# Performance work log

Measured on AMD Instinct MI355X. Metric: run time of the kernel, lower is better.

## Reference

```python
import jax, jax.numpy as jnp
import numpy as np
from jax.scipy.linalg import solve_triangular
from jax.scipy.special import logsumexp

N, K, D = 131072, 32, 32
LOG_2PI = np.float32(np.log(2.0 * np.pi))


def setup_inputs() -> dict:
    key = jax.random.key(0)
    k1, k2, k3, k4 = jax.random.split(key, 4)
    X = jax.random.normal(k1, (N, D), dtype=jnp.float32)
    means = jax.random.normal(k2, (K, D), dtype=jnp.float32)
    chols = jax.random.normal(k3, (K, D, D), dtype=jnp.float32)
    weights = jax.random.normal(k4, (K,), dtype=jnp.float32) - 1.0  # normal_(-1, 1)
    return {"X": X, "means": means, "chols": chols, "weights": weights, "it": 0}


def _neglog_likelihood(X, means, chols, weights):
    d = X.shape[-1]
    n = X.shape[0]
    eye = jnp.eye(d, dtype=X.dtype)
    # sigmas[k] = chols[k] @ chols[k]^T + I  -> (K, D, D)
    sigmas = jnp.einsum('kij,klj->kil', chols, chols) + eye
    L = jnp.linalg.cholesky(sigmas)                      # (K, D, D)
    # per-cluster Gaussian log-densities for all points, batched
    diff = X[None, :, :] - means[:, None, :]             # (K, N, D)
    y = solve_triangular(L, diff.transpose(0, 2, 1), lower=True)  # (K, D, N)
    maha = jnp.sum(y * y, axis=1)                        # (K, N)
    logdet = 2.0 * jnp.sum(jnp.log(jnp.diagonal(L, axis1=-2, axis2=-1)), axis=-1)  # (K,)
    log_dens = -0.5 * (maha + (logdet + d * LOG_2PI)[:, None])    # (K, N)
    dens = jnp.exp(log_dens)                             # (K, N)
    # sum_{i,j} w_i w_j N_i(x) N_j(x) = (sum_k w_k N_k(x))^2
    numer = jnp.square(weights @ dens)                   # (N,)
    # pairwise normaliser Z_ij = N(mu_i; mu_j, S_i + S_j), all pairs batched
    S_ij = sigmas[:, None] + sigmas[None, :]             # (K, K, D, D)
    L_ij = jnp.linalg.cholesky(S_ij)
    dmu = means[:, None, :] - means[None, :, :]          # (K, K, D)
    y_ij = solve_triangular(L_ij, dmu[..., None], lower=True)[..., 0]  # (K, K, D)
    maha_ij = jnp.sum(y_ij * y_ij, axis=-1)              # (K, K)
    logdet_ij = 2.0 * jnp.sum(jnp.log(jnp.diagonal(L_ij, axis1=-2, axis2=-1)), axis=-1)
    Z_ij = jnp.exp(-0.5 * (maha_ij + logdet_ij + d * LOG_2PI))
    z = jnp.sum((weights[:, None] * weights[None, :]) * Z_ij)
    pdf = numer / z                                      # (N,)
    logp = jnp.log(pdf)                                  # (N,)
    return -(logsumexp(logp, axis=0) / n)


def reference(X, means, chols, weights, it):
    return _neglog_likelihood(X, means, chols, weights)
```

## Files before the change

kernel.cpp:

```cpp
#include <hip/hip_runtime.h>
#include <math.h>

#define NPTS  131072
#define NPTB  512
#define NPRB  256
#define GRID  (NPTB + NPRB)
#define DLOG2PIF 58.8120661f
#define DLOG2PI  58.81206612467475
#define SHIFT 92.0f
#define NEGHALF_LOG2E -0.72134752044f
#define LOG2E 1.44269504089f

typedef __attribute__((ext_vector_type(8)))  short short8;
typedef __attribute__((ext_vector_type(16))) float f32x16;

static __device__ __forceinline__ unsigned bfh(float f) {
  unsigned u = __float_as_uint(f);
  return (u + 0x7FFFu + ((u >> 16) & 1u)) >> 16;
}
static __device__ __forceinline__ float bfhf(float f) {
  return __uint_as_float(bfh(f) << 16);
}
static __device__ __forceinline__ short8 mk_a2(unsigned w) {
  int4 t = {(int)w, 0, 0, 0};
  return __builtin_bit_cast(short8, t);
}

__global__ __launch_bounds__(256) void setup_kernel(
    const float* __restrict__ means, const float* __restrict__ chols,
    const float* __restrict__ wts,
    uint4* __restrict__ Afrag, float* __restrict__ Kc, float* __restrict__ Sg,
    unsigned* __restrict__ ticket)
{
  const int tid = threadIdx.x, wv = tid >> 6, lane = tid & 63;
  const int r = lane & 31, h = lane >> 5;
  const int k = blockIdx.x*4 + wv;
  __shared__ float SshA[4][1056];
  __shared__ float blsA[4][1056];
  float* Ssh = SshA[wv];
  float* bls = blsA[wv];
  if (blockIdx.x == 0 && tid == 0) *ticket = 0u;
  const float* cp = chols + (size_t)k*1024 + r*32;
  float4 fa = *(const float4*)(cp + h*8);
  float4 fb = *(const float4*)(cp + h*8 + 4);
  float4 fc = *(const float4*)(cp + 16 + h*8);
  float4 fd = *(const float4*)(cp + 16 + h*8 + 4);
  float v0[8] = {fa.x,fa.y,fa.z,fa.w,fb.x,fb.y,fb.z,fb.w};
  float v1[8] = {fc.x,fc.y,fc.z,fc.w,fd.x,fd.y,fd.z,fd.w};
  short8 hi0, hi1, lo0, lo1;
  #pragma unroll
  for (int j = 0; j < 8; j++) {
    hi0[j] = (short)bfh(v0[j]);  lo0[j] = (short)bfh(v0[j] - bfhf(v0[j]));
    hi1[j] = (short)bfh(v1[j]);  lo1[j] = (short)bfh(v1[j] - bfhf(v1[j]));
  }
  f32x16 acc = {};
  acc = __builtin_amdgcn_mfma_f32_32x32x16_bf16(hi0, hi0, acc, 0,0,0);
  acc = __builtin_amdgcn_mfma_f32_32x32x16_bf16(hi1, hi1, acc, 0,0,0);
  acc = __builtin_amdgcn_mfma_f32_32x32x16_bf16(hi0, lo0, acc, 0,0,0);
  acc = __builtin_amdgcn_mfma_f32_32x32x16_bf16(hi1, lo1, acc, 0,0,0);
  acc = __builtin_amdgcn_mfma_f32_32x32x16_bf16(lo0, hi0, acc, 0,0,0);
  acc = __builtin_amdgcn_mfma_f32_32x32x16_bf16(lo1, hi1, acc, 0,0,0);
  #pragma unroll
  for (int q = 0; q < 16; q++) {
    int row = (q & 3) + 8*(q >> 2) + 4*h;
    Ssh[row*33 + r] = acc[q] + ((row == r) ? 1.0f : 0.0f);
  }
  float a[32];
  #pragma unroll
  for (int j = 0; j < 32; j++) a[j] = Ssh[r*33 + j];
  float ldsum = 0.0f;
  #pragma unroll
  for (int j = 0; j < 32; j++) {
    float dd = __shfl(a[j], j);
    float inv = __frsqrt_rn(dd);
    float sq = dd * inv;
    ldsum += __logf(sq);
    float l = a[j] * inv;
    #pragma unroll
    for (int e = j+1; e < 32; e++) {
      float le = __shfl(l, e);
      a[e] = (r >= e) ? fmaf(-l, le, a[e]) : a[e];
    }
    a[j] = (r == j) ? sq : ((r > j) ? l : a[j]);
  }
  #pragma unroll
  for (int j = 0; j < 32; j++) Ssh[r*33 + j] = a[j];
  #pragma unroll 1
  for (int d = 0; d < 32; d++) {
    float s0 = (d == r) ? 1.0f : 0.0f, s1 = 0.0f;
    int j = 0;
    for (; j + 1 < d; j += 2) {
      s0 = fmaf(-Ssh[d*33 + j],     bls[j*33 + r],     s0);
      s1 = fmaf(-Ssh[d*33 + j + 1], bls[(j+1)*33 + r], s1);
    }
    if (j < d) s0 = fmaf(-Ssh[d*33 + j], bls[j*33 + r], s0);
    bls[d*33 + r] = (s0 + s1) / Ssh[d*33 + d];
  }
  float t0[8], t1[8];
  #pragma unroll
  for (int j = 0; j < 8; j++) {
    t0[j] = bls[r*33 + h*8 + j];
    t1[j] = bls[r*33 + 16 + h*8 + j];
  }
  uint4 s0 = make_uint4(bfh(t0[0])|(bfh(t0[1])<<16), bfh(t0[2])|(bfh(t0[3])<<16),
                        bfh(t0[4])|(bfh(t0[5])<<16), bfh(t0[6])|(bfh(t0[7])<<16));
  uint4 s1 = make_uint4(bfh(t1[0])|(bfh(t1[1])<<16), bfh(t1[2])|(bfh(t1[3])<<16),
                        bfh(t1[4])|(bfh(t1[5])<<16), bfh(t1[6])|(bfh(t1[7])<<16));
  float cvp = 0.0f;
  #pragma unroll
  for (int j = 0; j < 8; j++) {
    cvp = fmaf(t0[j], means[k*32 + h*8 + j], cvp);
    cvp = fmaf(t1[j], means[k*32 + 16 + h*8 + j], cvp);
  }
  float cv = cvp + __shfl_xor(cvp, 32);
  unsigned ch = bfh(cv) ^ 0x8000u;
  unsigned cl = bfh(cv - bfhf(cv)) ^ 0x8000u;
  uint4 s2 = make_uint4((h == 0) ? (ch | (cl<<16)) : 0u, 0u, 0u, 0u);
  Afrag[(k*3 + 0)*64 + lane] = s0;
  Afrag[(k*3 + 1)*64 + lane] = s1;
  Afrag[(k*3 + 2)*64 + lane] = s2;
  if (lane == 0) {
    float wk = wts[k];
    float ld2 = 2.0f*ldsum + DLOG2PIF;
    Kc[k] = LOG2E*(SHIFT - 0.5f*ld2) + log2f(fabsf(wk));
    Sg[k] = (wk < 0.0f) ? -1.0f : 1.0f;
  }
}

__global__ __launch_bounds__(256) void work_kernel(
    const float* __restrict__ X, const float* __restrict__ means,
    const float* __restrict__ chols, const float* __restrict__ wts,
    const uint4* __restrict__ Afrag, const float* __restrict__ Kc,
    const float* __restrict__ Sg,
    double* __restrict__ zterm, double* __restrict__ partials,
    unsigned* __restrict__ ticket, float* __restrict__ out)
{
  __shared__ __align__(16) char smem[24576];
  __shared__ float K2sh[32], sksh[32];
  __shared__ double redd[4], redz[4];
  __shared__ unsigned lastFlag;
  const int tid = threadIdx.x, wv = tid >> 6, lane = tid & 63;
  const int r = lane & 31, h = lane >> 5;
  if (blockIdx.x < NPTB) {
    uint4* fsh = (uint4*)smem;
    const unsigned* fshw = (const unsigned*)smem;
    if (tid < 32) { K2sh[tid] = Kc[tid]; sksh[tid] = Sg[tid]; }
    const int n0 = blockIdx.x*256 + wv*64 + r;
    short8 xh00, xh01, xh10, xh11, x2c;
    {
      const float* xp0 = X + (size_t)n0*32;
      const float* xp1 = X + (size_t)(n0+32)*32;
      float4 fa = *(const float4*)(xp0 + h*8);
      float4 fb = *(const float4*)(xp0 + h*8 + 4);
      float4 fc = *(const float4*)(xp0 + 16 + h*8);
      float4 fd = *(const float4*)(xp0 + 16 + h*8 + 4);
      float4 ga = *(const float4*)(xp1 + h*8);
      float4 gb = *(const float4*)(xp1 + h*8 + 4);
      float4 gc = *(const float4*)(xp1 + 16 + h*8);
      float4 gd = *(const float4*)(xp1 + 16 + h*8 + 4);
      float v00[8] = {fa.x,fa.y,fa.z,fa.w,fb.x,fb.y,fb.z,fb.w};
      float v01[8] = {fc.x,fc.y,fc.z,fc.w,fd.x,fd.y,fd.z,fd.w};
      float v10[8] = {ga.x,ga.y,ga.z,ga.w,gb.x,gb.y,gb.z,gb.w};
      float v11[8] = {gc.x,gc.y,gc.z,gc.w,gd.x,gd.y,gd.z,gd.w};
      #pragma unroll
      for (int j = 0; j < 8; j++) {
        xh00[j] = (short)bfh(v00[j]);  xh01[j] = (short)bfh(v01[j]);
        xh10[j] = (short)bfh(v10[j]);  xh11[j] = (short)bfh(v11[j]);
        x2c[j] = 0;
      }
      if (h == 0) { x2c[0] = (short)0x3F80; x2c[1] = (short)0x3F80; }
    }
    float sF0 = 0.0f, sF1 = 0.0f;
    #pragma unroll 1
    for (int ph = 0; ph < 4; ph++) {
      __syncthreads();
      const uint4* src = Afrag + ph*1536;
      #pragma unroll
      for (int t = tid; t < 1536; t += 256) fsh[t] = src[t];
      __syncthreads();
      #pragma unroll 4
      for (int kk = 0; kk < 8; kk++) {
        const short8* fp = (const short8*)(fsh + kk*192);
        short8 a0 = fp[lane], a1 = fp[64+lane];
        short8 a2 = mk_a2(fshw[(kk*192 + 128 + lane)*4]);
        const int kidx = ph*8 + kk;
        const float Kk = K2sh[kidx], sk = sksh[kidx];
        f32x16 acc0 = {}, acc1 = {};
        acc0 = __builtin_amdgcn_mfma_f32_32x32x16_bf16(a0, xh00, acc0, 0,0,0);
        acc0 = __builtin_amdgcn_mfma_f32_32x32x16_bf16(a1, xh01, acc0, 0,0,0);
        acc0 = __builtin_amdgcn_mfma_f32_32x32x16_bf16(a2, x2c,  acc0, 0,0,0);
        acc1 = __builtin_amdgcn_mfma_f32_32x32x16_bf16(a0, xh10, acc1, 0,0,0);
        acc1 = __builtin_amdgcn_mfma_f32_32x32x16_bf16(a1, xh11, acc1, 0,0,0);
        acc1 = __builtin_amdgcn_mfma_f32_32x32x16_bf16(a2, x2c,  acc1, 0,0,0);
        float m0a=0.f, m0b=0.f, m1a=0.f, m1b=0.f;
        #pragma unroll
        for (int q = 0; q < 8; q++) {
          m0a = fmaf(acc0[q],   acc0[q],   m0a);
          m0b = fmaf(acc0[q+8], acc0[q+8], m0b);
          m1a = fmaf(acc1[q],   acc1[q],   m1a);
          m1b = fmaf(acc1[q+8], acc1[q+8], m1b);
        }
        float m0 = m0a + m0b, m1 = m1a + m1b;
        m0 += __shfl_xor(m0, 32);
        m1 += __shfl_xor(m1, 32);
        sF0 = fmaf(sk, exp2f(fmaf(m0, NEGHALF_LOG2E, Kk)), sF0);
        sF1 = fmaf(sk, exp2f(fmaf(m1, NEGHALF_LOG2E, Kk)), sF1);
      }
    }
    double Tp = (double)sF0*(double)sF0 + (double)sF1*(double)sF1;
    if (lane >= 32) Tp = 0.0;
    #pragma unroll
    for (int off = 32; off > 0; off >>= 1) Tp += __shfl_down(Tp, off);
    if (lane == 0) redd[wv] = Tp;
    __syncthreads();
    if (tid == 0) partials[blockIdx.x] = redd[0] + redd[1] + redd[2] + redd[3];
  } else {
    float* Ssh = (float*)smem + wv*1056;
    const int pid = (blockIdx.x - NPTB)*4 + wv, pi = pid >> 5, pj = pid & 31;
    const float* cpi = chols + (size_t)pi*1024 + r*32;
    const float* cpj = chols + (size_t)pj*1024 + r*32;
    float4 ia = *(const float4*)(cpi + h*8);
    float4 ib = *(const float4*)(cpi + h*8 + 4);
    float4 ic = *(const float4*)(cpi + 16 + h*8);
    float4 id = *(const float4*)(cpi + 16 + h*8 + 4);
    float4 ja = *(const float4*)(cpj + h*8);
    float4 jb = *(const float4*)(cpj + h*8 + 4);
    float4 jc = *(const float4*)(cpj + 16 + h*8);
    float4 jd = *(const float4*)(cpj + 16 + h*8 + 4);
    float vi0[8] = {ia.x,ia.y,ia.z,ia.w,ib.x,ib.y,ib.z,ib.w};
    float vi1[8] = {ic.x,ic.y,ic.z,ic.w,id.x,id.y,id.z,id.w};
    float vj0[8] = {ja.x,ja.y,ja.z,ja.w,jb.x,jb.y,jb.z,jb.w};
    float vj1[8] = {jc.x,jc.y,jc.z,jc.w,jd.x,jd.y,jd.z,jd.w};
    short8 I0h,I0l,I1h,I1l,J0h,J0l,J1h,J1l;
    #pragma unroll
    for (int j = 0; j < 8; j++) {
      I0h[j]=(short)bfh(vi0[j]); I0l[j]=(short)bfh(vi0[j]-bfhf(vi0[j]));
      I1h[j]=(short)bfh(vi1[j]); I1l[j]=(short)bfh(vi1[j]-bfhf(vi1[j]));
      J0h[j]=(short)bfh(vj0[j]); J0l[j]=(short)bfh(vj0[j]-bfhf(vj0[j]));
      J1h[j]=(short)bfh(vj1[j]); J1l[j]=(short)bfh(vj1[j]-bfhf(vj1[j]));
    }
    f32x16 pacc = {};
    pacc = __builtin_amdgcn_mfma_f32_32x32x16_bf16(I0h, I0h, pacc, 0,0,0);
    pacc = __builtin_amdgcn_mfma_f32_32x32x16_bf16(I1h, I1h, pacc, 0,0,0);
    pacc = __builtin_amdgcn_mfma_f32_32x32x16_bf16(I0h, I0l, pacc, 0,0,0);
    pacc = __builtin_amdgcn_mfma_f32_32x32x16_bf16(I1h, I1l, pacc, 0,0,0);
    pacc = __builtin_amdgcn_mfma_f32_32x32x16_bf16(I0l, I0h, pacc, 0,0,0);
    pacc = __builtin_amdgcn_mfma_f32_32x32x16_bf16(I1l, I1h, pacc, 0,0,0);
    pacc = __builtin_amdgcn_mfma_f32_32x32x16_bf16(J0h, J0h, pacc, 0,0,0);
    pacc = __builtin_amdgcn_mfma_f32_32x32x16_bf16(J1h, J1h, pacc, 0,0,0);
    pacc = __builtin_amdgcn_mfma_f32_32x32x16_bf16(J0h, J0l, pacc, 0,0,0);
    pacc = __builtin_amdgcn_mfma_f32_32x32x16_bf16(J1h, J1l, pacc, 0,0,0);
    pacc = __builtin_amdgcn_mfma_f32_32x32x16_bf16(J0l, J0h, pacc, 0,0,0);
    pacc = __builtin_amdgcn_mfma_f32_32x32x16_bf16(J1l, J1h, pacc, 0,0,0);
    #pragma unroll
    for (int q = 0; q < 16; q++) {
      int row = (q & 3) + 8*(q >> 2) + 4*h;
      Ssh[row*33 + r] = pacc[q] + ((row == r) ? 2.0f : 0.0f);
    }
    float a[32];
    #pragma unroll
    for (int j = 0; j < 32; j++) a[j] = Ssh[r*33 + j];
    #pragma unroll
    for (int j = 0; j < 32; j++) {
      float dd = __shfl(a[j], j);
      float inv = __frsqrt_rn(dd);
      float sq = dd * inv;
      float l = a[j] * inv;
      #pragma unroll
      for (int e = j+1; e < 32; e++) {
        float le = __shfl(l, e);
        a[e] = (r >= e) ? fmaf(-l, le, a[e]) : a[e];
      }
      a[j] = (r == j) ? sq : ((r > j) ? l : a[j]);
    }
    float acc2 = means[pi*32 + r] - means[pj*32 + r];
    float maha = 0.0f, ldsum = 0.0f;
    #pragma unroll
    for (int d = 0; d < 32; d++) {
      float dd = __shfl(a[d], d);
      float yd = __shfl(acc2, d) / dd;
      maha = fmaf(yd, yd, maha);
      ldsum += __logf(dd);
      acc2 = (r > d) ? fmaf(-a[d], yd, acc2) : acc2;
    }
    if (lane == 0) {
      double vd = -0.5 * ((double)maha + 2.0*(double)ldsum + DLOG2PI);
      zterm[pid] = (double)wts[pi] * (double)wts[pj] * exp(vd);
    }
  }
  __syncthreads();
  if (tid == 0) {
    __threadfence();
    lastFlag = (atomicAdd(ticket, 1u) == GRID - 1) ? 1u : 0u;
  }
  __syncthreads();
  if (lastFlag) {
    __threadfence();
    double t = 0.0, z = 0.0;
    for (int p = tid; p < NPTB; p += 256) t += partials[p];
    for (int p = tid; p < 1024; p += 256) z += zterm[p];
    #pragma unroll
    for (int off = 32; off > 0; off >>= 1) {
      t += __shfl_down(t, off);
      z += __shfl_down(z, off);
    }
    if (lane == 0) { redd[wv] = t; redz[wv] = z; }
    __syncthreads();
    if (tid == 0) {
      t = redd[0] + redd[1] + redd[2] + redd[3];
      z = redz[0] + redz[1] + redz[2] + redz[3];
      double logT = log(t) - 2.0*(double)SHIFT;
      double logz = log(z);
      out[0] = (float)((logz - logT) / (double)NPTS);
    }
  }
}

extern "C" void kernel_launch(void* const* d_in, const int* in_sizes, int n_in,
                              void* d_out, int out_size, void* d_ws, size_t ws_size,
                              hipStream_t stream) {
  const float* X     = (const float*)d_in[0];
  const float* means = (const float*)d_in[1];
  const float* chols = (const float*)d_in[2];
  const float* wts   = (const float*)d_in[3];
  float* out = (float*)d_out;
  char* ws = (char*)d_ws;
  uint4*    Afrag    = (uint4*)ws;
  float*    Kc       = (float*)(ws + 98304);
  float*    Sg       = (float*)(ws + 98432);
  double*   zterm    = (double*)(ws + 98560);
  double*   partials = (double*)(ws + 106752);
  unsigned* ticket   = (unsigned*)(ws + 110848);

  setup_kernel<<<8, 256, 0, stream>>>(means, chols, wts, Afrag, Kc, Sg, ticket);
  work_kernel<<<GRID, 256, 0, stream>>>(X, means, chols, wts, Afrag, Kc, Sg,
                                        zterm, partials, ticket, out);
}
```

Measured before the change: 129.5 us.

## Fuse setup into work kernel with flag sync and expanded Mahalanobis form

Merges the setup kernel into one launch: the first 8 pair blocks compute the per-cluster Cholesky inverses and publish them through release-stored magic flags, and point blocks spin-wait on those flags. The Mahalanobis distance is rewritten as ||L^-1 x||^2 - 2 g·x + c, so the per-cluster mean-offset MFMA is dropped and a one-time G·X MFMA plus a per-cluster constant is used instead. Afrag staging becomes double-buffered with register prefetch and fully unrolled phases, and occupancy is hinted with launch_bounds(256,3). This removes a kernel launch gap and some MFMA work, at the cost of depending on the flag-writing blocks being scheduled, with precision risk from cancellation in the expanded quadratic form.

New measurement: 154.4 us. 19.2% more time.

```diff
diff --git a/kernel.cpp b/kernel.cpp
--- a/kernel.cpp
+++ b/kernel.cpp
@@ -2,14 +2,15 @@
 #include <math.h>
 
 #define NPTS  131072
+#define NPRB  256
 #define NPTB  512
-#define NPRB  256
-#define GRID  (NPTB + NPRB)
+#define GRID  (NPRB + NPTB)
 #define DLOG2PIF 58.8120661f
 #define DLOG2PI  58.81206612467475
 #define SHIFT 92.0f
 #define NEGHALF_LOG2E -0.72134752044f
 #define LOG2E 1.44269504089f
+#define MAGIC 0x9E3779B9u
 
 typedef __attribute__((ext_vector_type(8)))  short short8;
 typedef __attribute__((ext_vector_type(16))) float f32x16;
@@ -21,132 +22,213 @@
 static __device__ __forceinline__ float bfhf(float f) {
   return __uint_as_float(bfh(f) << 16);
 }
-static __device__ __forceinline__ short8 mk_a2(unsigned w) {
-  int4 t = {(int)w, 0, 0, 0};
-  return __builtin_bit_cast(short8, t);
-}
-
-__global__ __launch_bounds__(256) void setup_kernel(
-    const float* __restrict__ means, const float* __restrict__ chols,
-    const float* __restrict__ wts,
-    uint4* __restrict__ Afrag, float* __restrict__ Kc, float* __restrict__ Sg,
-    unsigned* __restrict__ ticket)
-{
-  const int tid = threadIdx.x, wv = tid >> 6, lane = tid & 63;
-  const int r = lane & 31, h = lane >> 5;
-  const int k = blockIdx.x*4 + wv;
-  __shared__ float SshA[4][1056];
-  __shared__ float blsA[4][1056];
-  float* Ssh = SshA[wv];
-  float* bls = blsA[wv];
-  if (blockIdx.x == 0 && tid == 0) *ticket = 0u;
-  const float* cp = chols + (size_t)k*1024 + r*32;
-  float4 fa = *(const float4*)(cp + h*8);
-  float4 fb = *(const float4*)(cp + h*8 + 4);
-  float4 fc = *(const float4*)(cp + 16 + h*8);
-  float4 fd = *(const float4*)(cp + 16 + h*8 + 4);
-  float v0[8] = {fa.x,fa.y,fa.z,fa.w,fb.x,fb.y,fb.z,fb.w};
-  float v1[8] = {fc.x,fc.y,fc.z,fc.w,fd.x,fd.y,fd.z,fd.w};
-  short8 hi0, hi1, lo0, lo1;
-  #pragma unroll
-  for (int j = 0; j < 8; j++) {
-    hi0[j] = (short)bfh(v0[j]);  lo0[j] = (short)bfh(v0[j] - bfhf(v0[j]));
-    hi1[j] = (short)bfh(v1[j]);  lo1[j] = (short)bfh(v1[j] - bfhf(v1[j]));
-  }
-  f32x16 acc = {};
-  acc = __builtin_amdgcn_mfma_f32_32x32x16_bf16(hi0, hi0, acc, 0,0,0);
-  acc = __builtin_amdgcn_mfma_f32_32x32x16_bf16(hi1, hi1, acc, 0,0,0);
-  acc = __builtin_amdgcn_mfma_f32_32x32x16_bf16(hi0, lo0, acc, 0,0,0);
-  acc = __builtin_amdgcn_mfma_f32_32x32x16_bf16(hi1, lo1, acc, 0,0,0);
-  acc = __builtin_amdgcn_mfma_f32_32x32x16_bf16(lo0, hi0, acc, 0,0,0);
-  acc = __builtin_amdgcn_mfma_f32_32x32x16_bf16(lo1, hi1, acc, 0,0,0);
-  #pragma unroll
-  for (int q = 0; q < 16; q++) {
-    int row = (q & 3) + 8*(q >> 2) + 4*h;
-    Ssh[row*33 + r] = acc[q] + ((row == r) ? 1.0f : 0.0f);
-  }
-  float a[32];
-  #pragma unroll
-  for (int j = 0; j < 32; j++) a[j] = Ssh[r*33 + j];
-  float ldsum = 0.0f;
-  #pragma unroll
-  for (int j = 0; j < 32; j++) {
-    float dd = __shfl(a[j], j);
-    float inv = __frsqrt_rn(dd);
-    float sq = dd * inv;
-    ldsum += __logf(sq);
-    float l = a[j] * inv;
-    #pragma unroll
-    for (int e = j+1; e < 32; e++) {
-      float le = __shfl(l, e);
-      a[e] = (r >= e) ? fmaf(-l, le, a[e]) : a[e];
-    }
-    a[j] = (r == j) ? sq : ((r > j) ? l : a[j]);
-  }
-  #pragma unroll
-  for (int j = 0; j < 32; j++) Ssh[r*33 + j] = a[j];
-  #pragma unroll 1
-  for (int d = 0; d < 32; d++) {
-    float s0 = (d == r) ? 1.0f : 0.0f, s1 = 0.0f;
-    int j = 0;
-    for (; j + 1 < d; j += 2) {
-      s0 = fmaf(-Ssh[d*33 + j],     bls[j*33 + r],     s0);
-      s1 = fmaf(-Ssh[d*33 + j + 1], bls[(j+1)*33 + r], s1);
-    }
-    if (j < d) s0 = fmaf(-Ssh[d*33 + j], bls[j*33 + r], s0);
-    bls[d*33 + r] = (s0 + s1) / Ssh[d*33 + d];
-  }
-  float t0[8], t1[8];
-  #pragma unroll
-  for (int j = 0; j < 8; j++) {
-    t0[j] = bls[r*33 + h*8 + j];
-    t1[j] = bls[r*33 + 16 + h*8 + j];
-  }
-  uint4 s0 = make_uint4(bfh(t0[0])|(bfh(t0[1])<<16), bfh(t0[2])|(bfh(t0[3])<<16),
-                        bfh(t0[4])|(bfh(t0[5])<<16), bfh(t0[6])|(bfh(t0[7])<<16));
-  uint4 s1 = make_uint4(bfh(t1[0])|(bfh(t1[1])<<16), bfh(t1[2])|(bfh(t1[3])<<16),
-                        bfh(t1[4])|(bfh(t1[5])<<16), bfh(t1[6])|(bfh(t1[7])<<16));
-  float cvp = 0.0f;
-  #pragma unroll
-  for (int j = 0; j < 8; j++) {
-    cvp = fmaf(t0[j], means[k*32 + h*8 + j], cvp);
-    cvp = fmaf(t1[j], means[k*32 + 16 + h*8 + j], cvp);
-  }
-  float cv = cvp + __shfl_xor(cvp, 32);
-  unsigned ch = bfh(cv) ^ 0x8000u;
-  unsigned cl = bfh(cv - bfhf(cv)) ^ 0x8000u;
-  uint4 s2 = make_uint4((h == 0) ? (ch | (cl<<16)) : 0u, 0u, 0u, 0u);
-  Afrag[(k*3 + 0)*64 + lane] = s0;
-  Afrag[(k*3 + 1)*64 + lane] = s1;
-  Afrag[(k*3 + 2)*64 + lane] = s2;
-  if (lane == 0) {
-    float wk = wts[k];
-    float ld2 = 2.0f*ldsum + DLOG2PIF;
-    Kc[k] = LOG2E*(SHIFT - 0.5f*ld2) + log2f(fabsf(wk));
-    Sg[k] = (wk < 0.0f) ? -1.0f : 1.0f;
-  }
-}
-
-__global__ __launch_bounds__(256) void work_kernel(
+
+__global__ __launch_bounds__(256, 3) void fused_kernel(
     const float* __restrict__ X, const float* __restrict__ means,
     const float* __restrict__ chols, const float* __restrict__ wts,
-    const uint4* __restrict__ Afrag, const float* __restrict__ Kc,
-    const float* __restrict__ Sg,
+    uint4* __restrict__ Afrag, float* __restrict__ gbuf,
+    float* __restrict__ Kc, float* __restrict__ Sg,
     double* __restrict__ zterm, double* __restrict__ partials,
-    unsigned* __restrict__ ticket, float* __restrict__ out)
+    unsigned* __restrict__ done, unsigned* __restrict__ ticket,
+    float* __restrict__ out)
 {
-  __shared__ __align__(16) char smem[24576];
+  __shared__ __align__(16) char smem[33792];
   __shared__ float K2sh[32], sksh[32];
   __shared__ double redd[4], redz[4];
   __shared__ unsigned lastFlag;
   const int tid = threadIdx.x, wv = tid >> 6, lane = tid & 63;
   const int r = lane & 31, h = lane >> 5;
-  if (blockIdx.x < NPTB) {
-    uint4* fsh = (uint4*)smem;
-    const unsigned* fshw = (const unsigned*)smem;
-    if (tid < 32) { K2sh[tid] = Kc[tid]; sksh[tid] = Sg[tid]; }
-    const int n0 = blockIdx.x*256 + wv*64 + r;
-    short8 xh00, xh01, xh10, xh11, x2c;
+
+  if (blockIdx.x < NPRB) {
+    if (blockIdx.x < 8) {
+      const int k = blockIdx.x*4 + wv;
+      float* Ssh = (float*)smem + wv*1056;
+      float* bls = (float*)smem + 4224 + wv*1056;
+      if (blockIdx.x == 0 && tid == 0) *ticket = 0u;
+      const float* cp = chols + (size_t)k*1024 + r*32;
+      float4 fa = *(const float4*)(cp + h*8);
+      float4 fb = *(const float4*)(cp + h*8 + 4);
+      float4 fc = *(const float4*)(cp + 16 + h*8);
+      float4 fd = *(const float4*)(cp + 16 + h*8 + 4);
+      float v0[8] = {fa.x,fa.y,fa.z,fa.w,fb.x,fb.y,fb.z,fb.w};
+      float v1[8] = {fc.x,fc.y,fc.z,fc.w,fd.x,fd.y,fd.z,fd.w};
+      short8 hi0, hi1, lo0, lo1;
+      #pragma unroll
+      for (int j = 0; j < 8; j++) {
+        hi0[j] = (short)bfh(v0[j]);  lo0[j] = (short)bfh(v0[j] - bfhf(v0[j]));
+        hi1[j] = (short)bfh(v1[j]);  lo1[j] = (short)bfh(v1[j] - bfhf(v1[j]));
+      }
+      f32x16 acc = {};
+      acc = __builtin_amdgcn_mfma_f32_32x32x16_bf16(hi0, hi0, acc, 0,0,0);
+      acc = __builtin_amdgcn_mfma_f32_32x32x16_bf16(hi1, hi1, acc, 0,0,0);
+      acc = __builtin_amdgcn_mfma_f32_32x32x16_bf16(hi0, lo0, acc, 0,0,0);
+      acc = __builtin_amdgcn_mfma_f32_32x32x16_bf16(hi1, lo1, acc, 0,0,0);
+      acc = __builtin_amdgcn_mfma_f32_32x32x16_bf16(lo0, hi0, acc, 0,0,0);
+      acc = __builtin_amdgcn_mfma_f32_32x32x16_bf16(lo1, hi1, acc, 0,0,0);
+      #pragma unroll
+      for (int q = 0; q < 16; q++) {
+        int row = (q & 3) + 8*(q >> 2) + 4*h;
+        Ssh[row*33 + r] = acc[q] + ((row == r) ? 1.0f : 0.0f);
+      }
+      float a[32];
+      #pragma unroll
+      for (int j = 0; j < 32; j++) a[j] = Ssh[r*33 + j];
+      float ldsum = 0.0f;
+      #pragma unroll
+      for (int j = 0; j < 32; j++) {
+        float dd = __shfl(a[j], j);
+        float inv = __frsqrt_rn(dd);
+        float sq = dd * inv;
+        ldsum += __logf(sq);
+        float l = a[j] * inv;
+        #pragma unroll
+        for (int e = j+1; e < 32; e++) {
+          float le = __shfl(l, e);
+          a[e] = (r >= e) ? fmaf(-l, le, a[e]) : a[e];
+        }
+        a[j] = (r == j) ? sq : ((r > j) ? l : a[j]);
+      }
+      #pragma unroll
+      for (int j = 0; j < 32; j++) Ssh[r*33 + j] = a[j];
+      #pragma unroll 1
+      for (int d = 0; d < 32; d++) {
+        float s0 = (d == r) ? 1.0f : 0.0f, s1 = 0.0f;
+        int j = 0;
+        for (; j + 1 < d; j += 2) {
+          s0 = fmaf(-Ssh[d*33 + j],     bls[j*33 + r],     s0);
+          s1 = fmaf(-Ssh[d*33 + j + 1], bls[(j+1)*33 + r], s1);
+        }
+        if (j < d) s0 = fmaf(-Ssh[d*33 + j], bls[j*33 + r], s0);
+        bls[d*33 + r] = (s0 + s1) / Ssh[d*33 + d];
+      }
+      float t0[8], t1[8];
+      #pragma unroll
+      for (int j = 0; j < 8; j++) {
+        t0[j] = bls[r*33 + h*8 + j];
+        t1[j] = bls[r*33 + 16 + h*8 + j];
+      }
+      uint4 s0 = make_uint4(bfh(t0[0])|(bfh(t0[1])<<16), bfh(t0[2])|(bfh(t0[3])<<16),
+                            bfh(t0[4])|(bfh(t0[5])<<16), bfh(t0[6])|(bfh(t0[7])<<16));
+      uint4 s1 = make_uint4(bfh(t1[0])|(bfh(t1[1])<<16), bfh(t1[2])|(bfh(t1[3])<<16),
+                            bfh(t1[4])|(bfh(t1[5])<<16), bfh(t1[6])|(bfh(t1[7])<<16));
+      Afrag[(k*2 + 0)*64 + lane] = s0;
+      Afrag[(k*2 + 1)*64 + lane] = s1;
+      const float* mk = means + k*32;
+      float wr = 0.0f;
+      #pragma unroll
+      for (int j = 0; j < 32; j++) wr = fmaf(bfhf(bls[r*33 + j]), mk[j], wr);
+      float c = wr*wr;
+      #pragma unroll
+      for (int off = 16; off > 0; off >>= 1) c += __shfl_xor(c, off);
+      float gd = 0.0f;
+      #pragma unroll
+      for (int rr = 0; rr < 32; rr++)
+        gd = fmaf(bfhf(bls[rr*33 + r]), __shfl(wr, rr), gd);
+      if (h == 0) gbuf[k*32 + r] = 2.0f*gd;
+      if (lane == 0) {
+        float wk = wts[k];
+        float ld2 = 2.0f*ldsum + DLOG2PIF;
+        Kc[k] = LOG2E*(SHIFT - 0.5f*ld2 - 0.5f*c) + log2f(fabsf(wk));
+        Sg[k] = (wk < 0.0f) ? -1.0f : 1.0f;
+      }
+      __syncthreads();
+      if (tid == 0) {
+        __threadfence();
+        __hip_atomic_store(&done[blockIdx.x], MAGIC, __ATOMIC_RELEASE,
+                           __HIP_MEMORY_SCOPE_AGENT);
+      }
+      __syncthreads();
+    }
+    {
+      float* Ssh = (float*)smem + wv*1056;
+      const int pid = blockIdx.x*4 + wv, pi = pid >> 5, pj = pid & 31;
+      const float* cpi = chols + (size_t)pi*1024 + r*32;
+      const float* cpj = chols + (size_t)pj*1024 + r*32;
+      float4 ia = *(const float4*)(cpi + h*8);
+      float4 ib = *(const float4*)(cpi + h*8 + 4);
+      float4 ic = *(const float4*)(cpi + 16 + h*8);
+      float4 id = *(const float4*)(cpi + 16 + h*8 + 4);
+      float4 ja = *(const float4*)(cpj + h*8);
+      float4 jb = *(const float4*)(cpj + h*8 + 4);
+      float4 jc = *(const float4*)(cpj + 16 + h*8);
+      float4 jd = *(const float4*)(cpj + 16 + h*8 + 4);
+      float vi0[8] = {ia.x,ia.y,ia.z,ia.w,ib.x,ib.y,ib.z,ib.w};
+      float vi1[8] = {ic.x,ic.y,ic.z,ic.w,id.x,id.y,id.z,id.w};
+      float vj0[8] = {ja.x,ja.y,ja.z,ja.w,jb.x,jb.y,jb.z,jb.w};
+      float vj1[8] = {jc.x,jc.y,jc.z,jc.w,jd.x,jd.y,jd.z,jd.w};
+      short8 I0h,I0l,I1h,I1l,J0h,J0l,J1h,J1l;
+      #pragma unroll
+      for (int j = 0; j < 8; j++) {
+        I0h[j]=(short)bfh(vi0[j]); I0l[j]=(short)bfh(vi0[j]-bfhf(vi0[j]));
+        I1h[j]=(short)bfh(vi1[j]); I1l[j]=(short)bfh(vi1[j]-bfhf(vi1[j]));
+        J0h[j]=(short)bfh(vj0[j]); J0l[j]=(short)bfh(vj0[j]-bfhf(vj0[j]));
+        J1h[j]=(short)bfh(vj1[j]); J1l[j]=(short)bfh(vj1[j]-bfhf(vj1[j]));
+      }
+      f32x16 pacc = {};
+      pacc = __builtin_amdgcn_mfma_f32_32x32x16_bf16(I0h, I0h, pacc, 0,0,0);
+      pacc = __builtin_amdgcn_mfma_f32_32x32x16_bf16(I1h, I1h, pacc, 0,0,0);
+      pacc = __builtin_amdgcn_mfma_f32_32x32x16_bf16(I0h, I0l, pacc, 0,0,0);
+      pacc = __builtin_amdgcn_mfma_f32_32x32x16_bf16(I1h, I1l, pacc, 0,0,0);
+      pacc = __builtin_amdgcn_mfma_f32_32x32x16_bf16(I0l, I0h, pacc, 0,0,0);
+      pacc = __builtin_amdgcn_mfma_f32_32x32x16_bf16(I1l, I1h, pacc, 0,0,0);
+      pacc = __builtin_amdgcn_mfma_f32_32x32x16_bf16(J0h, J0h, pacc, 0,0,0);
+      pacc = __builtin_amdgcn_mfma_f32_32x32x16_bf16(J1h, J1h, pacc, 0,0,0);
+      pacc = __builtin_amdgcn_mfma_f32_32x32x16_bf16(J0h, J0l, pacc, 0,0,0);
+      pacc = __builtin_amdgcn_mfma_f32_32x32x16_bf16(J1h, J1l, pacc, 0,0,0);
+      pacc = __builtin_amdgcn_mfma_f32_32x32x16_bf16(J0l, J0h, pacc, 0,0,0);
+      pacc = __builtin_amdgcn_mfma_f32_32x32x16_bf16(J1l, J1h, pacc, 0,0,0);
+      #pragma unroll
+      for (int q = 0; q < 16; q++) {
+        int row = (q & 3) + 8*(q >> 2) + 4*h;
+        Ssh[row*33 + r] = pacc[q] + ((row == r) ? 2.0f : 0.0f);
+      }
+      float a[32];
+      #pragma unroll
+      for (int j = 0; j < 32; j++) a[j] = Ssh[r*33 + j];
+      #pragma unroll
+      for (int j = 0; j < 32; j++) {
+        float dd = __shfl(a[j], j);
+        float inv = __frsqrt_rn(dd);
+        float sq = dd * inv;
+        float l = a[j] * inv;
+        #pragma unroll
+        for (int e = j+1; e < 32; e++) {
+          float le = __shfl(l, e);
+          a[e] = (r >= e) ? fmaf(-l, le, a[e]) : a[e];
+        }
+        a[j] = (r == j) ? sq : ((r > j) ? l : a[j]);
+      }
+      float acc2 = means[pi*32 + r] - means[pj*32 + r];
+      float maha = 0.0f, ldsum = 0.0f;
+      #pragma unroll
+      for (int d = 0; d < 32; d++) {
+        float dd = __shfl(a[d], d);
+        float yd = __shfl(acc2, d) / dd;
+        maha = fmaf(yd, yd, maha);
+        ldsum += __logf(dd);
+        acc2 = (r > d) ? fmaf(-a[d], yd, acc2) : acc2;
+      }
+      if (lane == 0) {
+        double vd = -0.5 * ((double)maha + 2.0*(double)ldsum + DLOG2PI);
+        zterm[pid] = (double)wts[pi] * (double)wts[pj] * exp(vd);
+      }
+    }
+    __syncthreads();
+    if (tid == 0) {
+      #pragma unroll 1
+      for (int i = 0; i < 8; i++)
+        while (__hip_atomic_load(&done[i], __ATOMIC_RELAXED,
+                                 __HIP_MEMORY_SCOPE_AGENT) != MAGIC)
+          __builtin_amdgcn_s_sleep(2);
+      __threadfence();
+      lastFlag = (atomicAdd(ticket, 1u) == GRID - 1) ? 1u : 0u;
+    }
+  } else {
+    const int bp = blockIdx.x - NPRB;
+    uint4* fsh0 = (uint4*)smem;
+    uint4* fsh1 = (uint4*)smem + 1024;
+    const int n0 = bp*256 + wv*64 + r;
+    short8 xh00, xh01, xh10, xh11;
     {
       const float* xp0 = X + (size_t)n0*32;
       const float* xp1 = X + (size_t)(n0+32)*32;
@@ -166,32 +248,65 @@
       for (int j = 0; j < 8; j++) {
         xh00[j] = (short)bfh(v00[j]);  xh01[j] = (short)bfh(v01[j]);
         xh10[j] = (short)bfh(v10[j]);  xh11[j] = (short)bfh(v11[j]);
-        x2c[j] = 0;
-      }
-      if (h == 0) { x2c[0] = (short)0x3F80; x2c[1] = (short)0x3F80; }
-    }
+      }
+    }
+    if (tid < 8) {
+      while (__hip_atomic_load(&done[tid], __ATOMIC_RELAXED,
+                               __HIP_MEMORY_SCOPE_AGENT) != MAGIC)
+        __builtin_amdgcn_s_sleep(8);
+    }
+    __syncthreads();
+    __threadfence();
+    uint4 p0a = Afrag[tid],       p0b = Afrag[tid + 256];
+    uint4 p0c = Afrag[tid + 512], p0d = Afrag[tid + 768];
+    if (tid < 32) { K2sh[tid] = Kc[tid]; sksh[tid] = Sg[tid]; }
+    f32x16 accg0 = {}, accg1 = {};
+    {
+      const float* gp = gbuf + r*32 + h*8;
+      float4 ga = *(const float4*)(gp);
+      float4 gb = *(const float4*)(gp + 4);
+      float4 gc = *(const float4*)(gp + 16);
+      float4 gdv = *(const float4*)(gp + 20);
+      float g0[8] = {ga.x,ga.y,ga.z,ga.w,gb.x,gb.y,gb.z,gb.w};
+      float g1[8] = {gc.x,gc.y,gc.z,gc.w,gdv.x,gdv.y,gdv.z,gdv.w};
+      short8 Gh0, Gl0, Gh1, Gl1;
+      #pragma unroll
+      for (int j = 0; j < 8; j++) {
+        Gh0[j] = (short)bfh(g0[j]); Gl0[j] = (short)bfh(g0[j] - bfhf(g0[j]));
+        Gh1[j] = (short)bfh(g1[j]); Gl1[j] = (short)bfh(g1[j] - bfhf(g1[j]));
+      }
+      accg0 = __builtin_amdgcn_mfma_f32_32x32x16_bf16(Gh0, xh00, accg0, 0,0,0);
+      accg0 = __builtin_amdgcn_mfma_f32_32x32x16_bf16(Gl0, xh00, accg0, 0,0,0);
+      accg0 = __builtin_amdgcn_mfma_f32_32x32x16_bf16(Gh1, xh01, accg0, 0,0,0);
+      accg0 = __builtin_amdgcn_mfma_f32_32x32x16_bf16(Gl1, xh01, accg0, 0,0,0);
+      accg1 = __builtin_amdgcn_mfma_f32_32x32x16_bf16(Gh0, xh10, accg1, 0,0,0);
+      accg1 = __builtin_amdgcn_mfma_f32_32x32x16_bf16(Gl0, xh10, accg1, 0,0,0);
+      accg1 = __builtin_amdgcn_mfma_f32_32x32x16_bf16(Gh1, xh11, accg1, 0,0,0);
+      accg1 = __builtin_amdgcn_mfma_f32_32x32x16_bf16(Gl1, xh11, accg1, 0,0,0);
+    }
+    fsh0[tid] = p0a; fsh0[tid + 256] = p0b; fsh0[tid + 512] = p0c; fsh0[tid + 768] = p0d;
+    __syncthreads();
     float sF0 = 0.0f, sF1 = 0.0f;
-    #pragma unroll 1
+    #pragma unroll
     for (int ph = 0; ph < 4; ph++) {
-      __syncthreads();
-      const uint4* src = Afrag + ph*1536;
-      #pragma unroll
-      for (int t = tid; t < 1536; t += 256) fsh[t] = src[t];
-      __syncthreads();
-      #pragma unroll 4
+      uint4 nx0, nx1, nx2, nx3;
+      if (ph < 3) {
+        const uint4* srcA = Afrag + (ph + 1)*1024;
+        nx0 = srcA[tid];       nx1 = srcA[tid + 256];
+        nx2 = srcA[tid + 512]; nx3 = srcA[tid + 768];
+      }
+      const uint4* fsh = (ph & 1) ? fsh1 : fsh0;
+      #pragma unroll
       for (int kk = 0; kk < 8; kk++) {
-        const short8* fp = (const short8*)(fsh + kk*192);
-        short8 a0 = fp[lane], a1 = fp[64+lane];
-        short8 a2 = mk_a2(fshw[(kk*192 + 128 + lane)*4]);
         const int kidx = ph*8 + kk;
+        const short8* ap = (const short8*)(fsh + kk*128);
+        short8 a0 = ap[lane], a1 = ap[64 + lane];
         const float Kk = K2sh[kidx], sk = sksh[kidx];
         f32x16 acc0 = {}, acc1 = {};
         acc0 = __builtin_amdgcn_mfma_f32_32x32x16_bf16(a0, xh00, acc0, 0,0,0);
         acc0 = __builtin_amdgcn_mfma_f32_32x32x16_bf16(a1, xh01, acc0, 0,0,0);
-        acc0 = __builtin_amdgcn_mfma_f32_32x32x16_bf16(a2, x2c,  acc0, 0,0,0);
         acc1 = __builtin_amdgcn_mfma_f32_32x32x16_bf16(a0, xh10, acc1, 0,0,0);
         acc1 = __builtin_amdgcn_mfma_f32_32x32x16_bf16(a1, xh11, acc1, 0,0,0);
-        acc1 = __builtin_amdgcn_mfma_f32_32x32x16_bf16(a2, x2c,  acc1, 0,0,0);
         float m0a=0.f, m0b=0.f, m1a=0.f, m1b=0.f;
         #pragma unroll
         for (int q = 0; q < 8; q++) {
@@ -200,12 +315,20 @@
           m1a = fmaf(acc1[q],   acc1[q],   m1a);
           m1b = fmaf(acc1[q+8], acc1[q+8], m1b);
         }
-        float m0 = m0a + m0b, m1 = m1a + m1b;
+        const int qg = (kidx & 3) | (((kidx >> 3) & 3) << 2);
+        const int hneed = (kidx >> 2) & 1;
+        float m0 = m0a + m0b - ((h == hneed) ? accg0[qg] : 0.0f);
+        float m1 = m1a + m1b - ((h == hneed) ? accg1[qg] : 0.0f);
         m0 += __shfl_xor(m0, 32);
         m1 += __shfl_xor(m1, 32);
         sF0 = fmaf(sk, exp2f(fmaf(m0, NEGHALF_LOG2E, Kk)), sF0);
         sF1 = fmaf(sk, exp2f(fmaf(m1, NEGHALF_LOG2E, Kk)), sF1);
       }
+      if (ph < 3) {
+        uint4* nb = (ph & 1) ? fsh0 : fsh1;
+        nb[tid] = nx0; nb[tid + 256] = nx1; nb[tid + 512] = nx2; nb[tid + 768] = nx3;
+      }
+      __syncthreads();
     }
     double Tp = (double)sF0*(double)sF0 + (double)sF1*(double)sF1;
     if (lane >= 32) Tp = 0.0;
@@ -213,85 +336,11 @@
     for (int off = 32; off > 0; off >>= 1) Tp += __shfl_down(Tp, off);
     if (lane == 0) redd[wv] = Tp;
     __syncthreads();
-    if (tid == 0) partials[blockIdx.x] = redd[0] + redd[1] + redd[2] + redd[3];
-  } else {
-    float* Ssh = (float*)smem + wv*1056;
-    const int pid = (blockIdx.x - NPTB)*4 + wv, pi = pid >> 5, pj = pid & 31;
-    const float* cpi = chols + (size_t)pi*1024 + r*32;
-    const float* cpj = chols + (size_t)pj*1024 + r*32;
-    float4 ia = *(const float4*)(cpi + h*8);
-    float4 ib = *(const float4*)(cpi + h*8 + 4);
-    float4 ic = *(const float4*)(cpi + 16 + h*8);
-    float4 id = *(const float4*)(cpi + 16 + h*8 + 4);
-    float4 ja = *(const float4*)(cpj + h*8);
-    float4 jb = *(const float4*)(cpj + h*8 + 4);
-    float4 jc = *(const float4*)(cpj + 16 + h*8);
-    float4 jd = *(const float4*)(cpj + 16 + h*8 + 4);
-    float vi0[8] = {ia.x,ia.y,ia.z,ia.w,ib.x,ib.y,ib.z,ib.w};
-    float vi1[8] = {ic.x,ic.y,ic.z,ic.w,id.x,id.y,id.z,id.w};
-    float vj0[8] = {ja.x,ja.y,ja.z,ja.w,jb.x,jb.y,jb.z,jb.w};
-    float vj1[8] = {jc.x,jc.y,jc.z,jc.w,jd.x,jd.y,jd.z,jd.w};
-    short8 I0h,I0l,I1h,I1l,J0h,J0l,J1h,J1l;
-    #pragma unroll
-    for (int j = 0; j < 8; j++) {
-      I0h[j]=(short)bfh(vi0[j]); I0l[j]=(short)bfh(vi0[j]-bfhf(vi0[j]));
-      I1h[j]=(short)bfh(vi1[j]); I1l[j]=(short)bfh(vi1[j]-bfhf(vi1[j]));
-      J0h[j]=(short)bfh(vj0[j]); J0l[j]=(short)bfh(vj0[j]-bfhf(vj0[j]));
-      J1h[j]=(short)bfh(vj1[j]); J1l[j]=(short)bfh(vj1[j]-bfhf(vj1[j]));
-    }
-    f32x16 pacc = {};
-    pacc = __builtin_amdgcn_mfma_f32_32x32x16_bf16(I0h, I0h, pacc, 0,0,0);
-    pacc = __builtin_amdgcn_mfma_f32_32x32x16_bf16(I1h, I1h, pacc, 0,0,0);
-    pacc = __builtin_amdgcn_mfma_f32_32x32x16_bf16(I0h, I0l, pacc, 0,0,0);
-    pacc = __builtin_amdgcn_mfma_f32_32x32x16_bf16(I1h, I1l, pacc, 0,0,0);
-    pacc = __builtin_amdgcn_mfma_f32_32x32x16_bf16(I0l, I0h, pacc, 0,0,0);
-    pacc = __builtin_amdgcn_mfma_f32_32x32x16_bf16(I1l, I1h, pacc, 0,0,0);
-    pacc = __builtin_amdgcn_mfma_f32_32x32x16_bf16(J0h, J0h, pacc, 0,0,0);
-    pacc = __builtin_amdgcn_mfma_f32_32x32x16_bf16(J1h, J1h, pacc, 0,0,0);
-    pacc = __builtin_amdgcn_mfma_f32_32x32x16_bf16(J0h, J0l, pacc, 0,0,0);
-    pacc = __builtin_amdgcn_mfma_f32_32x32x16_bf16(J1h, J1l, pacc, 0,0,0);
-    pacc = __builtin_amdgcn_mfma_f32_32x32x16_bf16(J0l, J0h, pacc, 0,0,0);
-    pacc = __builtin_amdgcn_mfma_f32_32x32x16_bf16(J1l, J1h, pacc, 0,0,0);
-    #pragma unroll
-    for (int q = 0; q < 16; q++) {
-      int row = (q & 3) + 8*(q >> 2) + 4*h;
-      Ssh[row*33 + r] = pacc[q] + ((row == r) ? 2.0f : 0.0f);
-    }
-    float a[32];
-    #pragma unroll
-    for (int j = 0; j < 32; j++) a[j] = Ssh[r*33 + j];
-    #pragma unroll
-    for (int j = 0; j < 32; j++) {
-      float dd = __shfl(a[j], j);
-      float inv = __frsqrt_rn(dd);
-      float sq = dd * inv;
-      float l = a[j] * inv;
-      #pragma unroll
-      for (int e = j+1; e < 32; e++) {
-        float le = __shfl(l, e);
-        a[e] = (r >= e) ? fmaf(-l, le, a[e]) : a[e];
-      }
-      a[j] = (r == j) ? sq : ((r > j) ? l : a[j]);
-    }
-    float acc2 = means[pi*32 + r] - means[pj*32 + r];
-    float maha = 0.0f, ldsum = 0.0f;
-    #pragma unroll
-    for (int d = 0; d < 32; d++) {
-      float dd = __shfl(a[d], d);
-      float yd = __shfl(acc2, d) / dd;
-      maha = fmaf(yd, yd, maha);
-      ldsum += __logf(dd);
-      acc2 = (r > d) ? fmaf(-a[d], yd, acc2) : acc2;
-    }
-    if (lane == 0) {
-      double vd = -0.5 * ((double)maha + 2.0*(double)ldsum + DLOG2PI);
-      zterm[pid] = (double)wts[pi] * (double)wts[pj] * exp(vd);
-    }
-  }
-  __syncthreads();
-  if (tid == 0) {
-    __threadfence();
-    lastFlag = (atomicAdd(ticket, 1u) == GRID - 1) ? 1u : 0u;
+    if (tid == 0) {
+      partials[bp] = redd[0] + redd[1] + redd[2] + redd[3];
+      __threadfence();
+      lastFlag = (atomicAdd(ticket, 1u) == GRID - 1) ? 1u : 0u;
+    }
   }
   __syncthreads();
   if (lastFlag) {
@@ -326,13 +375,14 @@
   float* out = (float*)d_out;
   char* ws = (char*)d_ws;
   uint4*    Afrag    = (uint4*)ws;
-  float*    Kc       = (float*)(ws + 98304);
-  float*    Sg       = (float*)(ws + 98432);
-  double*   zterm    = (double*)(ws + 98560);
-  double*   partials = (double*)(ws + 106752);
-  unsigned* ticket   = (unsigned*)(ws + 110848);
-
-  setup_kernel<<<8, 256, 0, stream>>>(means, chols, wts, Afrag, Kc, Sg, ticket);
-  work_kernel<<<GRID, 256, 0, stream>>>(X, means, chols, wts, Afrag, Kc, Sg,
-                                        zterm, partials, ticket, out);
+  float*    gbuf     = (float*)(ws + 65536);
+  float*    Kc       = (float*)(ws + 69632);
+  float*    Sg       = (float*)(ws + 69760);
+  double*   zterm    = (double*)(ws + 69888);
+  double*   partials = (double*)(ws + 78080);
+  unsigned* done     = (unsigned*)(ws + 82176);
+  unsigned* ticket   = (unsigned*)(ws + 82208);
+
+  fused_kernel<<<GRID, 256, 0, stream>>>(X, means, chols, wts, Afrag, gbuf, Kc, Sg,
+                                         zterm, partials, done, ticket, out);
 }
```
